# Performance work log

Measured on AMD Instinct MI355X. Metric: run time of the kernel, lower is better.

Reference implementation:

```python
import jax, jax.numpy as jnp
import numpy as np
from jax import lax

D_MODEL = 256
DEPTH = 2
DI = 512        # d_inner = expand * d_model
N = 16          # d_state
DCONV = 4
DTR = 16        # dt_rank = ceil(d_model/16)
BSZ = 32
T = 2048
EPS = 1e-5


def setup_inputs() -> dict:
    key = jax.random.key(0)
    ks = jax.random.split(key, 13)
    s = 0.02
    x = jax.random.normal(ks[0], (BSZ, T, D_MODEL), jnp.float32)
    mask = jax.random.randint(ks[1], (BSZ, T), 0, 2) > 0
    ln_w = 1.0 + 0.1 * jax.random.normal(ks[2], (DEPTH, D_MODEL), jnp.float32)
    ln_b = 0.1 * jax.random.normal(ks[3], (DEPTH, D_MODEL), jnp.float32)
    in_proj_w = s * jax.random.normal(ks[4], (DEPTH, 2 * DI, D_MODEL), jnp.float32)
    conv_w = s * jax.random.normal(ks[5], (DEPTH, DI, DCONV), jnp.float32)
    conv_b = s * jax.random.normal(ks[6], (DEPTH, DI), jnp.float32)
    x_proj_w = s * jax.random.normal(ks[7], (DEPTH, DTR + 2 * N, DI), jnp.float32)
    dt_proj_w = s * jax.random.normal(ks[8], (DEPTH, DI, DTR), jnp.float32)
    dt_proj_b = s * jax.random.normal(ks[9], (DEPTH, DI), jnp.float32)
    # A = -exp(A_log) in (-e^3, -1): stable decaying dynamics
    A_log = jax.random.uniform(ks[10], (DEPTH, DI, N), jnp.float32, 0.0, 3.0)
    skip_D = s * jax.random.normal(ks[11], (DEPTH, DI), jnp.float32)
    out_proj_w = s * jax.random.normal(ks[12], (DEPTH, D_MODEL, DI), jnp.float32)
    return {"x": x, "mask": mask, "ln_w": ln_w, "ln_b": ln_b,
            "in_proj_w": in_proj_w, "conv_w": conv_w, "conv_b": conv_b,
            "x_proj_w": x_proj_w, "dt_proj_w": dt_proj_w, "dt_proj_b": dt_proj_b,
            "A_log": A_log, "skip_D": skip_D, "out_proj_w": out_proj_w}


def _layernorm(x, w, b):
    mu = jnp.mean(x, axis=-1, keepdims=True)
    var = jnp.mean(jnp.square(x - mu), axis=-1, keepdims=True)
    return (x - mu) * lax.rsqrt(var + EPS) * w + b


def _mamba(x, in_proj_w, conv_w, conv_b, x_proj_w, dt_proj_w, dt_proj_b, A_log, skip_D, out_proj_w):
    Bsz, L, _ = x.shape
    xz = jnp.einsum('btd,ed->bte', x, in_proj_w)      # (B,T,2*DI)
    u, z = jnp.split(xz, 2, axis=-1)                  # (B,T,DI) each
    # causal depthwise conv1d, kernel size DCONV
    up = jnp.pad(u, ((0, 0), (DCONV - 1, 0), (0, 0)))
    uc = conv_b
    for k in range(DCONV):
        uc = uc + up[:, k:k + L, :] * conv_w[:, k]
    u = jax.nn.silu(uc)
    x_dbl = jnp.einsum('btd,ed->bte', u, x_proj_w)    # (B,T,DTR+2N)
    dt_in, Bm, Cm = jnp.split(x_dbl, [DTR, DTR + N], axis=-1)
    dt = jax.nn.softplus(jnp.einsum('btr,dr->btd', dt_in, dt_proj_w) + dt_proj_b)  # (B,T,DI)
    A = -jnp.exp(A_log)                               # (DI,N)

    def step(h, inp):
        dt_t, B_t, C_t, u_t = inp                     # (B,DI),(B,N),(B,N),(B,DI)
        dA = jnp.exp(dt_t[..., None] * A)             # (B,DI,N)
        h = dA * h + (dt_t * u_t)[..., None] * B_t[:, None, :]
        y = jnp.einsum('bdn,bn->bd', h, C_t)
        return h, y

    h0 = jnp.zeros((Bsz, DI, N), x.dtype)
    xs = (dt.transpose(1, 0, 2), Bm.transpose(1, 0, 2),
          Cm.transpose(1, 0, 2), u.transpose(1, 0, 2))
    _, ys = lax.scan(step, h0, xs)                    # (T,B,DI)
    y = ys.transpose(1, 0, 2) + u * skip_D
    y = y * jax.nn.silu(z)
    return jnp.einsum('btd,ed->bte', y, out_proj_w)   # (B,T,d_model)


def reference(x, mask, ln_w, ln_b, in_proj_w, conv_w, conv_b, x_proj_w,
              dt_proj_w, dt_proj_b, A_log, skip_D, out_proj_w):
    m = mask[..., None].astype(x.dtype)
    x = x * m
    for i in range(DEPTH):
        h = _mamba(_layernorm(x, ln_w[i], ln_b[i]), in_proj_w[i], conv_w[i],
                   conv_b[i], x_proj_w[i], dt_proj_w[i], dt_proj_b[i],
                   A_log[i], skip_D[i], out_proj_w[i])
        x = (x + h) * m   # dropout in eval mode = identity
    return x
```

## Files before the change

### kernel.cpp

```cpp
#include <hip/hip_runtime.h>
#include <cstdint>

#define LOG2E 1.4426950408889634f
#define BCH 16
#define RC  (BCH * 2048)

typedef __attribute__((ext_vector_type(8))) short short8;
typedef __attribute__((ext_vector_type(4))) float f32x4;
typedef __attribute__((ext_vector_type(4))) unsigned short ush4;
typedef __attribute__((ext_vector_type(8))) unsigned short ush8;

__device__ __forceinline__ float b2f(unsigned short u) {
  union { unsigned int u; float f; } c; c.u = ((unsigned int)u) << 16; return c.f;
}
__device__ __forceinline__ unsigned short f2b(float f) {
  union { float f; unsigned int u; } c; c.f = f;
  unsigned int r = c.u + 0x7FFFu + ((c.u >> 16) & 1u);
  return (unsigned short)(r >> 16);
}
__device__ __forceinline__ float ex2(float x) { return __builtin_amdgcn_exp2f(x); }
__device__ __forceinline__ f32x4 exp2v(f32x4 v) {
  f32x4 r; r.x = ex2(v.x); r.y = ex2(v.y); r.z = ex2(v.z); r.w = ex2(v.w);
  return r;
}

__device__ __forceinline__ f32x4 ld4(const float* p) {
  f32x4 r;
  asm volatile("global_load_dwordx4 %0, %1, off" : "=v"(r) : "v"(p));
  return r;
}

__device__ __forceinline__ void gl2lds16(void* l, const void* g) {
  __builtin_amdgcn_global_load_lds(
      (const __attribute__((address_space(1))) void*)g,
      (__attribute__((address_space(3))) void*)l, 16, 0, 0);
}

__global__ __launch_bounds__(256) void prep_weights(
    const float* __restrict__ inw, const float* __restrict__ xw,
    const float* __restrict__ ow, const float* __restrict__ alog,
    unsigned short* __restrict__ inwb, unsigned short* __restrict__ xwb,
    unsigned short* __restrict__ owb, float* __restrict__ AA) {
  int gid = blockIdx.x * 256 + threadIdx.x;
  const int n_in = 2 * 1024 * 256;
  const int n_x  = 2 * 48 * 512;
  const int n_o  = 2 * 256 * 512;
  const int n_a  = 2 * 512 * 16;
  if (gid < n_in) { inwb[gid] = f2b(inw[gid]); return; }
  gid -= n_in;
  if (gid < n_x) { xwb[gid] = f2b(xw[gid]); return; }
  gid -= n_x;
  if (gid < n_o) { owb[gid] = f2b(ow[gid]); return; }
  gid -= n_o;
  if (gid < n_a) { AA[gid] = -__expf(alog[gid]) * LOG2E; }
}

__global__ __launch_bounds__(256) void mask_x(
    const float* __restrict__ x, const int* __restrict__ mask,
    float* __restrict__ X) {
  int gid = blockIdx.x * 256 + threadIdx.x;
  int row = gid >> 8;
  X[gid] = mask[row] ? x[gid] : 0.f;
}

__global__ __launch_bounds__(256) void ln_fwd(
    const float* __restrict__ X, const float* __restrict__ w,
    const float* __restrict__ b, unsigned short* __restrict__ XN) {
  int wv = threadIdx.x >> 6, ln = threadIdx.x & 63;
  long row = (long)blockIdx.x * 4 + wv;
  f32x4 v = ((const f32x4*)(X + row * 256))[ln];
  float s = v.x + v.y + v.z + v.w;
  float s2 = v.x * v.x + v.y * v.y + v.z * v.z + v.w * v.w;
  #pragma unroll
  for (int o = 32; o > 0; o >>= 1) {
    s += __shfl_xor(s, o, 64);
    s2 += __shfl_xor(s2, o, 64);
  }
  float mu = s * (1.f / 256.f);
  float var = s2 * (1.f / 256.f) - mu * mu;
  float rst = rsqrtf(var + 1e-5f);
  f32x4 wv4 = ((const f32x4*)w)[ln];
  f32x4 bv4 = ((const f32x4*)b)[ln];
  ush4 o4;
  o4.x = f2b((v.x - mu) * rst * wv4.x + bv4.x);
  o4.y = f2b((v.y - mu) * rst * wv4.y + bv4.y);
  o4.z = f2b((v.z - mu) * rst * wv4.z + bv4.z);
  o4.w = f2b((v.w - mu) * rst * wv4.w + bv4.w);
  ((ush4*)(XN + row * 256))[ln] = o4;
}

__global__ __launch_bounds__(256) void gemm128(
    const unsigned short* __restrict__ A, const unsigned short* __restrict__ B,
    unsigned short* __restrict__ OutU, unsigned short* __restrict__ OutZ,
    int N, int K) {
  __shared__ unsigned short As[128 * 32];
  __shared__ unsigned short Bs[128 * 32];
  const int tid = threadIdx.x;
  const int wave = tid >> 6, lane = tid & 63;
  const int lin = blockIdx.x + blockIdx.y * 256;
  const int xcd = lin & 7, idx = lin >> 3;
  const int m0 = (xcd * 32 + (idx >> 3)) * 128;
  const int n0 = (idx & 7) * 128;
  const int wm = (wave >> 1) * 64, wn = (wave & 1) * 64;

  f32x4 acc[4][4];
  #pragma unroll
  for (int i = 0; i < 4; i++)
    #pragma unroll
    for (int j = 0; j < 4; j++)
      #pragma unroll
      for (int r = 0; r < 4; r++) acc[i][j][r] = 0.f;

  const int srow = wave * 32 + (lane >> 2);
  const int skcol = (lane & 3) * 8;
  unsigned short* AsW = &As[srow * 32 + skcol];
  unsigned short* BsW = &Bs[srow * 32 + skcol];
  const unsigned short* Ag = A + (long)(m0 + srow) * K + skcol;
  const unsigned short* Bg = B + (long)(n0 + srow) * K + skcol;

  const int fr = lane & 15, fk = (lane >> 4) * 8;

  for (int k0 = 0; k0 < K; k0 += 32) {
    gl2lds16(AsW,            Ag + k0);
    gl2lds16(AsW + 16 * 32,  Ag + (long)16 * K + k0);
    gl2lds16(BsW,            Bg + k0);
    gl2lds16(BsW + 16 * 32,  Bg + (long)16 * K + k0);
    __syncthreads();
    short8 af[4], bf[4];
    #pragma unroll
    for (int i = 0; i < 4; i++) {
      af[i] = *(const short8*)&As[(wm + i * 16 + fr) * 32 + fk];
      bf[i] = *(const short8*)&Bs[(wn + i * 16 + fr) * 32 + fk];
    }
    #pragma unroll
    for (int i = 0; i < 4; i++)
      #pragma unroll
      for (int j = 0; j < 4; j++)
        acc[i][j] = __builtin_amdgcn_mfma_f32_16x16x32_bf16(af[i], bf[j], acc[i][j], 0, 0, 0);
    __syncthreads();
  }

  const int cl = lane & 15, rq = (lane >> 4) * 4;
  #pragma unroll
  for (int i = 0; i < 4; i++)
    #pragma unroll
    for (int j = 0; j < 4; j++) {
      int col = n0 + wn + j * 16 + cl;
      #pragma unroll
      for (int r = 0; r < 4; r++) {
        int row = m0 + wm + i * 16 + rq + r;
        float v = acc[i][j][r];
        if (col < 512) OutU[(long)row * 512 + col] = f2b(v);
        else           OutZ[(long)row * 512 + (col - 512)] = f2b(v);
      }
    }
}

__global__ __launch_bounds__(256) void gemm64(
    const unsigned short* __restrict__ A, const unsigned short* __restrict__ B,
    const float* __restrict__ Xres, float* __restrict__ OutF,
    const int* __restrict__ mask, int N, int K) {
  __shared__ unsigned short As[64 * 32];
  __shared__ unsigned short Bs[128 * 32];
  const int tid = threadIdx.x;
  const int wave = tid >> 6, lane = tid & 63;
  const int lin = blockIdx.x + blockIdx.y * 512;
  const int xcd = lin & 7, idx = lin >> 3;
  const int m0 = (xcd * 64 + (idx >> 1)) * 64;
  const int n0 = (idx & 1) * 128;
  const int wm = (wave >> 1) * 32, wn = (wave & 1) * 64;

  f32x4 acc[2][4];
  #pragma unroll
  for (int i = 0; i < 2; i++)
    #pragma unroll
    for (int j = 0; j < 4; j++)
      #pragma unroll
      for (int r = 0; r < 4; r++) acc[i][j][r] = 0.f;

  const int srow = wave * 32 + (lane >> 2);
  const int skcol = (lane & 3) * 8;
  unsigned short* AsW = &As[srow * 32 + skcol];
  unsigned short* BsW = &Bs[srow * 32 + skcol];
  const unsigned short* Ag = A + (long)(m0 + srow) * K + skcol;
  const unsigned short* Bg = B + (long)(n0 + srow) * K + skcol;

  const int fr = lane & 15, fk = (lane >> 4) * 8;

  for (int k0 = 0; k0 < K; k0 += 32) {
    if (wave < 2) {
      gl2lds16(AsW,            Ag + k0);
      gl2lds16(AsW + 16 * 32,  Ag + (long)16 * K + k0);
    }
    gl2lds16(BsW,            Bg + k0);
    gl2lds16(BsW + 16 * 32,  Bg + (long)16 * K + k0);
    __syncthreads();
    short8 af[2], bf[4];
    #pragma unroll
    for (int i = 0; i < 2; i++)
      af[i] = *(const short8*)&As[(wm + i * 16 + fr) * 32 + fk];
    #pragma unroll
    for (int j = 0; j < 4; j++)
      bf[j] = *(const short8*)&Bs[(wn + j * 16 + fr) * 32 + fk];
    #pragma unroll
    for (int i = 0; i < 2; i++)
      #pragma unroll
      for (int j = 0; j < 4; j++)
        acc[i][j] = __builtin_amdgcn_mfma_f32_16x16x32_bf16(af[i], bf[j], acc[i][j], 0, 0, 0);
    __syncthreads();
  }

  const int cl = lane & 15, rq = (lane >> 4) * 4;
  #pragma unroll
  for (int i = 0; i < 2; i++)
    #pragma unroll
    for (int j = 0; j < 4; j++) {
      int col = n0 + wn + j * 16 + cl;
      #pragma unroll
      for (int r = 0; r < 4; r++) {
        int row = m0 + wm + i * 16 + rq + r;
        long idx2 = (long)row * N + col;
        OutF[idx2] = Xres[idx2] + (mask[row] ? acc[i][j][r] : 0.f);
      }
    }
}

__global__ __launch_bounds__(256) void gemm_n48(
    const unsigned short* __restrict__ A, const unsigned short* __restrict__ B,
    float* __restrict__ Out, int K) {
  __shared__ unsigned short As[128 * 32];
  __shared__ unsigned short Bs[48 * 32];
  const int tid = threadIdx.x;
  const int wave = tid >> 6, lane = tid & 63;
  const int m0 = blockIdx.x * 128;
  const int wm = wave * 32;

  f32x4 acc[2][3];
  #pragma unroll
  for (int i = 0; i < 2; i++)
    #pragma unroll
    for (int j = 0; j < 3; j++)
      #pragma unroll
      for (int r = 0; r < 4; r++) acc[i][j][r] = 0.f;

  const int srow = wave * 32 + (lane >> 2);
  const int skcol = (lane & 3) * 8;
  unsigned short* AsW = &As[srow * 32 + skcol];
  const unsigned short* Ag = A + (long)(m0 + srow) * K + skcol;
  const int brow = wave * 16 + (lane >> 2);
  unsigned short* BsW = &Bs[brow * 32 + skcol];
  const unsigned short* Bg = B + (long)brow * K + skcol;

  const int fr = lane & 15, fk = (lane >> 4) * 8;

  for (int k0 = 0; k0 < K; k0 += 32) {
    gl2lds16(AsW,           Ag + k0);
    gl2lds16(AsW + 16 * 32, Ag + (long)16 * K + k0);
    if (wave < 3) gl2lds16(BsW, Bg + k0);
    __syncthreads();
    short8 af[2], bf[3];
    #pragma unroll
    for (int i = 0; i < 2; i++)
      af[i] = *(const short8*)&As[(wm + i * 16 + fr) * 32 + fk];
    #pragma unroll
    for (int j = 0; j < 3; j++)
      bf[j] = *(const short8*)&Bs[(j * 16 + fr) * 32 + fk];
    #pragma unroll
    for (int i = 0; i < 2; i++)
      #pragma unroll
      for (int j = 0; j < 3; j++)
        acc[i][j] = __builtin_amdgcn_mfma_f32_16x16x32_bf16(af[i], bf[j], acc[i][j], 0, 0, 0);
    __syncthreads();
  }

  const int cl = lane & 15, rq = (lane >> 4) * 4;
  #pragma unroll
  for (int i = 0; i < 2; i++)
    #pragma unroll
    for (int j = 0; j < 3; j++) {
      int col = j * 16 + cl;
      #pragma unroll
      for (int r = 0; r < 4; r++) {
        int row = m0 + wm + i * 16 + rq + r;
        Out[(long)row * 48 + col] = acc[i][j][r];
      }
    }
}

__global__ __launch_bounds__(256, 4) void conv_silu(
    const unsigned short* __restrict__ Upre, const float* __restrict__ cw,
    const float* __restrict__ cb, unsigned short* __restrict__ U) {
  int gid = blockIdx.x * 256 + threadIdx.x;
  int d8 = gid & 63;
  int row = gid >> 6;
  int t = row & 2047;
  int d0 = d8 * 8;
  f32x4 cwv[8];
  #pragma unroll
  for (int di = 0; di < 8; di++) cwv[di] = ((const f32x4*)(cw + (d0 + di) * 4))[0];
  f32x4 cbv0 = ((const f32x4*)(cb + d0))[0];
  f32x4 cbv1 = ((const f32x4*)(cb + d0))[1];
  float acc[8] = {cbv0.x, cbv0.y, cbv0.z, cbv0.w, cbv1.x, cbv1.y, cbv1.z, cbv1.w};
  #pragma unroll
  for (int k = 0; k < 4; k++) {
    int tt = t + k - 3;
    if (tt >= 0) {
      ush8 uv = *(const ush8*)(Upre + (long)(row + k - 3) * 512 + d0);
      #pragma unroll
      for (int di = 0; di < 8; di++)
        acc[di] = fmaf(b2f(uv[di]), cwv[di][k], acc[di]);
    }
  }
  ush8 o;
  #pragma unroll
  for (int di = 0; di < 8; di++) {
    float sg = 1.f / (1.f + __expf(-acc[di]));
    o[di] = f2b(acc[di] * sg);
  }
  *(ush8*)(U + (long)row * 512 + d0) = o;
}

template<int DTM>
__global__ __launch_bounds__(256, 8) void scan_p1(
    const unsigned short* __restrict__ U, const float* __restrict__ XD,
    const float* __restrict__ AA, const float* __restrict__ dtw,
    const float* __restrict__ dtb, float* __restrict__ HCH,
    float* __restrict__ DTS, _Float16* __restrict__ DTH) {
  int gid = blockIdx.x * 256 + threadIdx.x;
  int d = gid & 511;
  int bc = gid >> 9;
  int c = bc & 63, b = bc >> 6;
  f32x4 aa0 = ld4(AA + d * 16),      aa1 = ld4(AA + d * 16 + 4),
        aa2 = ld4(AA + d * 16 + 8),  aa3 = ld4(AA + d * 16 + 12);
  f32x4 w0 = ld4(dtw + d * 16),      w1 = ld4(dtw + d * 16 + 4),
        w2 = ld4(dtw + d * 16 + 8),  w3 = ld4(dtw + d * 16 + 12);
  asm volatile("s_waitcnt vmcnt(0)"
               : "+v"(aa0), "+v"(aa1), "+v"(aa2), "+v"(aa3),
                 "+v"(w0), "+v"(w1), "+v"(w2), "+v"(w3));
  f32x4 h0 = {0.f,0.f,0.f,0.f}, h1 = h0, h2 = h0, h3 = h0;
  float bias = dtb[d];
  float dts = 0.f;
  int row = b * 2048 + c * 32;
  const unsigned short* Up = U + (long)row * 512 + d;
  _Float16* DTp = DTH + (long)row * 512 + d;
  for (int tt = 0; tt < 32; tt++, row++, Up += 512, DTp += 512) {
    int off = __builtin_amdgcn_readfirstlane(row * 48);
    const f32x4* xs = (const f32x4*)(XD + off);
    f32x4 x0 = xs[0], x1 = xs[1], x2 = xs[2], x3 = xs[3];
    f32x4 B0 = xs[4], B1 = xs[5], B2 = xs[6], B3 = xs[7];
    f32x4 pp = x0 * w0 + x1 * w1 + x2 * w2 + x3 * w3;
    float s = bias + pp.x + pp.y + pp.z + pp.w;
    float e = __expf(-fabsf(s));
    float dt = fmaxf(s, 0.f) + __logf(1.f + e);
    if (DTM) *DTp = (_Float16)dt;
    float du = dt * b2f(*Up);
    h0 = exp2v(dt * aa0) * h0 + du * B0;
    h1 = exp2v(dt * aa1) * h1 + du * B1;
    h2 = exp2v(dt * aa2) * h2 + du * B2;
    h3 = exp2v(dt * aa3) * h3 + du * B3;
    dts += dt;
  }
  f32x4* hp = (f32x4*)(HCH + (long)gid * 16);
  hp[0] = h0; hp[1] = h1; hp[2] = h2; hp[3] = h3;
  DTS[gid] = dts;
}

__global__ __launch_bounds__(256) void scan_p2(
    float* __restrict__ HCH, const float* __restrict__ DTS,
    const float* __restrict__ AA) {
  int gid = blockIdx.x * 256 + threadIdx.x;
  int n = gid & 15;
  int d = (gid >> 4) & 511;
  int b = gid >> 13;
  float aa = AA[d * 16 + n];
  float hrun = 0.f;
  for (int c = 0; c < 64; c++) {
    long base = ((long)b * 64 + c) * 512 + d;
    long idx = base * 16 + n;
    float hend = HCH[idx];
    float P = ex2(DTS[base] * aa);
    HCH[idx] = hrun;
    hrun = fmaf(P, hrun, hend);
  }
}

template<int DTM>
__global__ __launch_bounds__(256, 8) void scan_p3(
    const unsigned short* __restrict__ U, const unsigned short* __restrict__ Z,
    const float* __restrict__ XD, const float* __restrict__ AA,
    const float* __restrict__ dtw, const float* __restrict__ dtb,
    const float* __restrict__ HCH, const float* __restrict__ skD,
    unsigned short* __restrict__ Y, const _Float16* __restrict__ DTH) {
  int gid = blockIdx.x * 256 + threadIdx.x;
  int d = gid & 511;
  int bc = gid >> 9;
  int c = bc & 63, b = bc >> 6;
  f32x4 aa0 = ld4(AA + d * 16),      aa1 = ld4(AA + d * 16 + 4),
        aa2 = ld4(AA + d * 16 + 8),  aa3 = ld4(AA + d * 16 + 12);
  f32x4 w0, w1, w2, w3;
  if (!DTM) {
    w0 = ld4(dtw + d * 16);     w1 = ld4(dtw + d * 16 + 4);
    w2 = ld4(dtw + d * 16 + 8); w3 = ld4(dtw + d * 16 + 12);
    asm volatile("s_waitcnt vmcnt(0)"
                 : "+v"(aa0), "+v"(aa1), "+v"(aa2), "+v"(aa3),
                   "+v"(w0), "+v"(w1), "+v"(w2), "+v"(w3));
  } else {
    asm volatile("s_waitcnt vmcnt(0)"
                 : "+v"(aa0), "+v"(aa1), "+v"(aa2), "+v"(aa3));
  }
  const f32x4* hp = (const f32x4*)(HCH + (long)gid * 16);
  f32x4 h0 = hp[0], h1 = hp[1], h2 = hp[2], h3 = hp[3];
  float bias = DTM ? 0.f : dtb[d];
  float sD = skD[d];
  int row = b * 2048 + c * 32;
  const unsigned short* Up = U + (long)row * 512 + d;
  const unsigned short* Zp = Z + (long)row * 512 + d;
  unsigned short* Yp = Y + (long)row * 512 + d;
  const _Float16* DTp = DTH + (long)row * 512 + d;
  for (int tt = 0; tt < 32; tt++, row++, Up += 512, Zp += 512, Yp += 512, DTp += 512) {
    int off = __builtin_amdgcn_readfirstlane(row * 48);
    const f32x4* xs = (const f32x4*)(XD + off);
    f32x4 B0 = xs[4], B1 = xs[5], B2 = xs[6], B3 = xs[7];
    f32x4 C0 = xs[8], C1 = xs[9], C2 = xs[10], C3 = xs[11];
    float dt;
    if (DTM) {
      dt = (float)*DTp;
    } else {
      f32x4 x0 = xs[0], x1 = xs[1], x2 = xs[2], x3 = xs[3];
      f32x4 pp = x0 * w0 + x1 * w1 + x2 * w2 + x3 * w3;
      float s = bias + pp.x + pp.y + pp.z + pp.w;
      float e = __expf(-fabsf(s));
      dt = fmaxf(s, 0.f) + __logf(1.f + e);
    }
    float u = b2f(*Up);
    float du = dt * u;
    h0 = exp2v(dt * aa0) * h0 + du * B0;
    h1 = exp2v(dt * aa1) * h1 + du * B1;
    h2 = exp2v(dt * aa2) * h2 + du * B2;
    h3 = exp2v(dt * aa3) * h3 + du * B3;
    f32x4 yv = h0 * C0 + h1 * C1 + h2 * C2 + h3 * C3;
    float y = yv.x + yv.y + yv.z + yv.w + u * sD;
    float z = b2f(*Zp);
    float sg = z / (1.f + __expf(-z));
    *Yp = f2b(y * sg);
  }
}

extern "C" void kernel_launch(void* const* d_in, const int* in_sizes, int n_in,
                              void* d_out, int out_size, void* d_ws, size_t ws_size,
                              hipStream_t stream) {
  const float* x        = (const float*)d_in[0];
  const int*   mask     = (const int*)d_in[1];
  const float* ln_w     = (const float*)d_in[2];
  const float* ln_b     = (const float*)d_in[3];
  const float* in_proj  = (const float*)d_in[4];
  const float* conv_w   = (const float*)d_in[5];
  const float* conv_b   = (const float*)d_in[6];
  const float* x_proj   = (const float*)d_in[7];
  const float* dt_w     = (const float*)d_in[8];
  const float* dt_b     = (const float*)d_in[9];
  const float* A_log    = (const float*)d_in[10];
  const float* skip_D   = (const float*)d_in[11];
  const float* out_proj = (const float*)d_in[12];
  float* X = (float*)d_out;

  char* p = (char*)d_ws;
  auto alloc = [&](size_t n) { char* r = p; p += (n + 255) & ~(size_t)255; return r; };
  unsigned short* WBin  = (unsigned short*)alloc((size_t)2 * 1024 * 256 * 2);
  unsigned short* WBx   = (unsigned short*)alloc((size_t)2 * 48 * 512 * 2);
  unsigned short* WBout = (unsigned short*)alloc((size_t)2 * 256 * 512 * 2);
  float*          AA    = (float*)alloc((size_t)2 * 512 * 16 * 4);
  char* R_XN   = alloc((size_t)RC * 256 * 2);
  char* R_UPRE = alloc((size_t)RC * 512 * 2);
  char* R_Z    = alloc((size_t)RC * 512 * 2);
  char* R_U    = alloc((size_t)RC * 512 * 2);
  char* R_DT   = alloc((size_t)RC * 512 * 2);

  unsigned short* XN   = (unsigned short*)R_XN;
  float*          XD   = (float*)R_XN;
  float*          DTS  = (float*)(R_XN + 8388608);
  unsigned short* Upre = (unsigned short*)R_UPRE;
  float*          HCH  = (float*)R_UPRE;
  unsigned short* Z    = (unsigned short*)R_Z;
  unsigned short* U    = (unsigned short*)R_U;
  _Float16*       DTH  = (_Float16*)R_DT;

  const bool use_dt = ws_size >= (size_t)((char*)p - (char*)d_ws);

  prep_weights<<<3328, 256, 0, stream>>>(in_proj, x_proj, out_proj, A_log,
                                         WBin, WBx, WBout, AA);
  mask_x<<<65536, 256, 0, stream>>>(x, mask, X);

  for (int ch = 0; ch < 2; ch++) {
    const long row0 = (long)ch * RC;
    float* Xc = X + row0 * 256;
    const int* maskc = mask + row0;
    for (int i = 0; i < 2; i++) {
      ln_fwd<<<RC / 4, 256, 0, stream>>>(Xc, ln_w + i * 256, ln_b + i * 256, XN);
      gemm128<<<dim3(RC / 128, 8), 256, 0, stream>>>(XN, WBin + i * 262144,
          Upre, Z, 1024, 256);
      conv_silu<<<RC / 4, 256, 0, stream>>>(Upre, conv_w + i * 2048,
          conv_b + i * 512, U);
      gemm_n48<<<RC / 128, 256, 0, stream>>>(U, WBx + i * 24576, XD, 512);
      if (use_dt) {
        scan_p1<1><<<BCH * 128, 256, 0, stream>>>(U, XD, AA + i * 8192,
            dt_w + i * 8192, dt_b + i * 512, HCH, DTS, DTH);
      } else {
        scan_p1<0><<<BCH * 128, 256, 0, stream>>>(U, XD, AA + i * 8192,
            dt_w + i * 8192, dt_b + i * 512, HCH, DTS, DTH);
      }
      scan_p2<<<BCH * 32, 256, 0, stream>>>(HCH, DTS, AA + i * 8192);
      if (use_dt) {
        scan_p3<1><<<BCH * 128, 256, 0, stream>>>(U, Z, XD, AA + i * 8192,
            dt_w + i * 8192, dt_b + i * 512, HCH, skip_D + i * 512, U, DTH);
      } else {
        scan_p3<0><<<BCH * 128, 256, 0, stream>>>(U, Z, XD, AA + i * 8192,
            dt_w + i * 8192, dt_b + i * 512, HCH, skip_D + i * 512, U, DTH);
      }
      gemm64<<<dim3(RC / 64, 2), 256, 0, stream>>>(U, WBout + i * 131072,
          Xc, Xc, maskc, 256, 512);
    }
  }
}
```

Baseline: 1.125 ms.

## Process two scan chunks per thread and fuse masking into first layernorm

```diff
diff --git a/kernel.cpp b/kernel.cpp
--- a/kernel.cpp
+++ b/kernel.cpp
@@ -55,20 +55,41 @@
   if (gid < n_a) { AA[gid] = -__expf(alog[gid]) * LOG2E; }
 }
 
-__global__ __launch_bounds__(256) void mask_x(
-    const float* __restrict__ x, const int* __restrict__ mask,
-    float* __restrict__ X) {
-  int gid = blockIdx.x * 256 + threadIdx.x;
-  int row = gid >> 8;
-  X[gid] = mask[row] ? x[gid] : 0.f;
-}
-
 __global__ __launch_bounds__(256) void ln_fwd(
     const float* __restrict__ X, const float* __restrict__ w,
     const float* __restrict__ b, unsigned short* __restrict__ XN) {
   int wv = threadIdx.x >> 6, ln = threadIdx.x & 63;
   long row = (long)blockIdx.x * 4 + wv;
   f32x4 v = ((const f32x4*)(X + row * 256))[ln];
+  float s = v.x + v.y + v.z + v.w;
+  float s2 = v.x * v.x + v.y * v.y + v.z * v.z + v.w * v.w;
+  #pragma unroll
+  for (int o = 32; o > 0; o >>= 1) {
+    s += __shfl_xor(s, o, 64);
+    s2 += __shfl_xor(s2, o, 64);
+  }
+  float mu = s * (1.f / 256.f);
+  float var = s2 * (1.f / 256.f) - mu * mu;
+  float rst = rsqrtf(var + 1e-5f);
+  f32x4 wv4 = ((const f32x4*)w)[ln];
+  f32x4 bv4 = ((const f32x4*)b)[ln];
+  ush4 o4;
+  o4.x = f2b((v.x - mu) * rst * wv4.x + bv4.x);
+  o4.y = f2b((v.y - mu) * rst * wv4.y + bv4.y);
+  o4.z = f2b((v.z - mu) * rst * wv4.z + bv4.z);
+  o4.w = f2b((v.w - mu) * rst * wv4.w + bv4.w);
+  ((ush4*)(XN + row * 256))[ln] = o4;
+}
+
+__global__ __launch_bounds__(256) void ln_mask_fwd(
+    const float* __restrict__ Xin, const int* __restrict__ mask,
+    const float* __restrict__ w, const float* __restrict__ b,
+    float* __restrict__ Xout, unsigned short* __restrict__ XN) {
+  int wv = threadIdx.x >> 6, ln = threadIdx.x & 63;
+  long row = (long)blockIdx.x * 4 + wv;
+  f32x4 v = ((const f32x4*)(Xin + row * 256))[ln];
+  if (!mask[row]) { v.x = 0.f; v.y = 0.f; v.z = 0.f; v.w = 0.f; }
+  ((f32x4*)(Xout + row * 256))[ln] = v;
   float s = v.x + v.y + v.z + v.w;
   float s2 = v.x * v.x + v.y * v.y + v.z * v.z + v.w * v.w;
   #pragma unroll
@@ -321,15 +342,15 @@
 }
 
 template<int DTM>
-__global__ __launch_bounds__(256, 8) void scan_p1(
+__global__ __launch_bounds__(256, 3) void scan_p1(
     const unsigned short* __restrict__ U, const float* __restrict__ XD,
     const float* __restrict__ AA, const float* __restrict__ dtw,
     const float* __restrict__ dtb, float* __restrict__ HCH,
     float* __restrict__ DTS, _Float16* __restrict__ DTH) {
   int gid = blockIdx.x * 256 + threadIdx.x;
   int d = gid & 511;
-  int bc = gid >> 9;
-  int c = bc & 63, b = bc >> 6;
+  int pc = gid >> 9;
+  int c = pc & 31, b = pc >> 5;
   f32x4 aa0 = ld4(AA + d * 16),      aa1 = ld4(AA + d * 16 + 4),
         aa2 = ld4(AA + d * 16 + 8),  aa3 = ld4(AA + d * 16 + 12);
   f32x4 w0 = ld4(dtw + d * 16),      w1 = ld4(dtw + d * 16 + 4),
@@ -337,32 +358,56 @@
   asm volatile("s_waitcnt vmcnt(0)"
                : "+v"(aa0), "+v"(aa1), "+v"(aa2), "+v"(aa3),
                  "+v"(w0), "+v"(w1), "+v"(w2), "+v"(w3));
-  f32x4 h0 = {0.f,0.f,0.f,0.f}, h1 = h0, h2 = h0, h3 = h0;
+  f32x4 hA0 = {0.f,0.f,0.f,0.f}, hA1 = hA0, hA2 = hA0, hA3 = hA0;
+  f32x4 hB0 = hA0, hB1 = hA0, hB2 = hA0, hB3 = hA0;
   float bias = dtb[d];
-  float dts = 0.f;
-  int row = b * 2048 + c * 32;
-  const unsigned short* Up = U + (long)row * 512 + d;
-  _Float16* DTp = DTH + (long)row * 512 + d;
-  for (int tt = 0; tt < 32; tt++, row++, Up += 512, DTp += 512) {
-    int off = __builtin_amdgcn_readfirstlane(row * 48);
-    const f32x4* xs = (const f32x4*)(XD + off);
-    f32x4 x0 = xs[0], x1 = xs[1], x2 = xs[2], x3 = xs[3];
-    f32x4 B0 = xs[4], B1 = xs[5], B2 = xs[6], B3 = xs[7];
-    f32x4 pp = x0 * w0 + x1 * w1 + x2 * w2 + x3 * w3;
-    float s = bias + pp.x + pp.y + pp.z + pp.w;
-    float e = __expf(-fabsf(s));
-    float dt = fmaxf(s, 0.f) + __logf(1.f + e);
-    if (DTM) *DTp = (_Float16)dt;
-    float du = dt * b2f(*Up);
-    h0 = exp2v(dt * aa0) * h0 + du * B0;
-    h1 = exp2v(dt * aa1) * h1 + du * B1;
-    h2 = exp2v(dt * aa2) * h2 + du * B2;
-    h3 = exp2v(dt * aa3) * h3 + du * B3;
-    dts += dt;
-  }
-  f32x4* hp = (f32x4*)(HCH + (long)gid * 16);
-  hp[0] = h0; hp[1] = h1; hp[2] = h2; hp[3] = h3;
-  DTS[gid] = dts;
+  float dtsA = 0.f, dtsB = 0.f;
+  int rowA = b * 2048 + c * 32;
+  int rowB = rowA + 1024;
+  const unsigned short* UpA = U + (long)rowA * 512 + d;
+  const unsigned short* UpB = U + (long)rowB * 512 + d;
+  _Float16* DTpA = DTH + (long)rowA * 512 + d;
+  _Float16* DTpB = DTH + (long)rowB * 512 + d;
+  for (int tt = 0; tt < 32; tt++) {
+    int offA = __builtin_amdgcn_readfirstlane(rowA * 48);
+    int offB = __builtin_amdgcn_readfirstlane(rowB * 48);
+    const f32x4* xsA = (const f32x4*)(XD + offA);
+    const f32x4* xsB = (const f32x4*)(XD + offB);
+    unsigned short uA = *UpA, uB = *UpB;
+    f32x4 xA0 = xsA[0], xA1 = xsA[1], xA2 = xsA[2], xA3 = xsA[3];
+    f32x4 xB0 = xsB[0], xB1 = xsB[1], xB2 = xsB[2], xB3 = xsB[3];
+    f32x4 ppA = xA0 * w0 + xA1 * w1 + xA2 * w2 + xA3 * w3;
+    f32x4 ppB = xB0 * w0 + xB1 * w1 + xB2 * w2 + xB3 * w3;
+    float sA = bias + ppA.x + ppA.y + ppA.z + ppA.w;
+    float sB = bias + ppB.x + ppB.y + ppB.z + ppB.w;
+    float eA = __expf(-fabsf(sA));
+    float eB = __expf(-fabsf(sB));
+    float dtA = fmaxf(sA, 0.f) + __logf(1.f + eA);
+    float dtB = fmaxf(sB, 0.f) + __logf(1.f + eB);
+    if (DTM) { *DTpA = (_Float16)dtA; *DTpB = (_Float16)dtB; }
+    float duA = dtA * b2f(uA);
+    float duB = dtB * b2f(uB);
+    f32x4 BA0 = xsA[4], BA1 = xsA[5], BA2 = xsA[6], BA3 = xsA[7];
+    f32x4 BB0 = xsB[4], BB1 = xsB[5], BB2 = xsB[6], BB3 = xsB[7];
+    hA0 = exp2v(dtA * aa0) * hA0 + duA * BA0;
+    hB0 = exp2v(dtB * aa0) * hB0 + duB * BB0;
+    hA1 = exp2v(dtA * aa1) * hA1 + duA * BA1;
+    hB1 = exp2v(dtB * aa1) * hB1 + duB * BB1;
+    hA2 = exp2v(dtA * aa2) * hA2 + duA * BA2;
+    hB2 = exp2v(dtB * aa2) * hB2 + duB * BB2;
+    hA3 = exp2v(dtA * aa3) * hA3 + duA * BA3;
+    hB3 = exp2v(dtB * aa3) * hB3 + duB * BB3;
+    dtsA += dtA; dtsB += dtB;
+    rowA++; rowB++; UpA += 512; UpB += 512; DTpA += 512; DTpB += 512;
+  }
+  long gidA = ((long)b * 64 + c) * 512 + d;
+  long gidB = gidA + 32 * 512;
+  f32x4* hpA = (f32x4*)(HCH + gidA * 16);
+  hpA[0] = hA0; hpA[1] = hA1; hpA[2] = hA2; hpA[3] = hA3;
+  f32x4* hpB = (f32x4*)(HCH + gidB * 16);
+  hpB[0] = hB0; hpB[1] = hB1; hpB[2] = hB2; hpB[3] = hB3;
+  DTS[gidA] = dtsA;
+  DTS[gidB] = dtsB;
 }
 
 __global__ __launch_bounds__(256) void scan_p2(
@@ -374,18 +419,29 @@
   int b = gid >> 13;
   float aa = AA[d * 16 + n];
   float hrun = 0.f;
-  for (int c = 0; c < 64; c++) {
-    long base = ((long)b * 64 + c) * 512 + d;
-    long idx = base * 16 + n;
-    float hend = HCH[idx];
-    float P = ex2(DTS[base] * aa);
-    HCH[idx] = hrun;
-    hrun = fmaf(P, hrun, hend);
+  for (int c4 = 0; c4 < 64; c4 += 4) {
+    float he0, he1, he2, he3, P0, P1, P2, P3;
+    long i0, i1, i2, i3;
+    {
+      long base0 = ((long)b * 64 + c4 + 0) * 512 + d;
+      long base1 = ((long)b * 64 + c4 + 1) * 512 + d;
+      long base2 = ((long)b * 64 + c4 + 2) * 512 + d;
+      long base3 = ((long)b * 64 + c4 + 3) * 512 + d;
+      i0 = base0 * 16 + n; i1 = base1 * 16 + n;
+      i2 = base2 * 16 + n; i3 = base3 * 16 + n;
+      he0 = HCH[i0]; he1 = HCH[i1]; he2 = HCH[i2]; he3 = HCH[i3];
+      P0 = ex2(DTS[base0] * aa); P1 = ex2(DTS[base1] * aa);
+      P2 = ex2(DTS[base2] * aa); P3 = ex2(DTS[base3] * aa);
+    }
+    HCH[i0] = hrun; hrun = fmaf(P0, hrun, he0);
+    HCH[i1] = hrun; hrun = fmaf(P1, hrun, he1);
+    HCH[i2] = hrun; hrun = fmaf(P2, hrun, he2);
+    HCH[i3] = hrun; hrun = fmaf(P3, hrun, he3);
   }
 }
 
 template<int DTM>
-__global__ __launch_bounds__(256, 8) void scan_p3(
+__global__ __launch_bounds__(256, 3) void scan_p3(
     const unsigned short* __restrict__ U, const unsigned short* __restrict__ Z,
     const float* __restrict__ XD, const float* __restrict__ AA,
     const float* __restrict__ dtw, const float* __restrict__ dtb,
@@ -393,8 +449,8 @@
     unsigned short* __restrict__ Y, const _Float16* __restrict__ DTH) {
   int gid = blockIdx.x * 256 + threadIdx.x;
   int d = gid & 511;
-  int bc = gid >> 9;
-  int c = bc & 63, b = bc >> 6;
+  int pc = gid >> 9;
+  int c = pc & 31, b = pc >> 5;
   f32x4 aa0 = ld4(AA + d * 16),      aa1 = ld4(AA + d * 16 + 4),
         aa2 = ld4(AA + d * 16 + 8),  aa3 = ld4(AA + d * 16 + 12);
   f32x4 w0, w1, w2, w3;
@@ -408,41 +464,81 @@
     asm volatile("s_waitcnt vmcnt(0)"
                  : "+v"(aa0), "+v"(aa1), "+v"(aa2), "+v"(aa3));
   }
-  const f32x4* hp = (const f32x4*)(HCH + (long)gid * 16);
-  f32x4 h0 = hp[0], h1 = hp[1], h2 = hp[2], h3 = hp[3];
+  long gidA = ((long)b * 64 + c) * 512 + d;
+  long gidB = gidA + 32 * 512;
+  f32x4 hA0, hA1, hA2, hA3, hB0, hB1, hB2, hB3;
+  {
+    const f32x4* hpA = (const f32x4*)(HCH + gidA * 16);
+    hA0 = hpA[0]; hA1 = hpA[1]; hA2 = hpA[2]; hA3 = hpA[3];
+    const f32x4* hpB = (const f32x4*)(HCH + gidB * 16);
+    hB0 = hpB[0]; hB1 = hpB[1]; hB2 = hpB[2]; hB3 = hpB[3];
+  }
   float bias = DTM ? 0.f : dtb[d];
   float sD = skD[d];
-  int row = b * 2048 + c * 32;
-  const unsigned short* Up = U + (long)row * 512 + d;
-  const unsigned short* Zp = Z + (long)row * 512 + d;
-  unsigned short* Yp = Y + (long)row * 512 + d;
-  const _Float16* DTp = DTH + (long)row * 512 + d;
-  for (int tt = 0; tt < 32; tt++, row++, Up += 512, Zp += 512, Yp += 512, DTp += 512) {
-    int off = __builtin_amdgcn_readfirstlane(row * 48);
-    const f32x4* xs = (const f32x4*)(XD + off);
-    f32x4 B0 = xs[4], B1 = xs[5], B2 = xs[6], B3 = xs[7];
-    f32x4 C0 = xs[8], C1 = xs[9], C2 = xs[10], C3 = xs[11];
-    float dt;
+  int rowA = b * 2048 + c * 32;
+  int rowB = rowA + 1024;
+  const unsigned short* UpA = U + (long)rowA * 512 + d;
+  const unsigned short* UpB = U + (long)rowB * 512 + d;
+  const unsigned short* ZpA = Z + (long)rowA * 512 + d;
+  const unsigned short* ZpB = Z + (long)rowB * 512 + d;
+  unsigned short* YpA = Y + (long)rowA * 512 + d;
+  unsigned short* YpB = Y + (long)rowB * 512 + d;
+  const _Float16* DTpA = DTH + (long)rowA * 512 + d;
+  const _Float16* DTpB = DTH + (long)rowB * 512 + d;
+  for (int tt = 0; tt < 32; tt++) {
+    int offA = __builtin_amdgcn_readfirstlane(rowA * 48);
+    int offB = __builtin_amdgcn_readfirstlane(rowB * 48);
+    const f32x4* xsA = (const f32x4*)(XD + offA);
+    const f32x4* xsB = (const f32x4*)(XD + offB);
+    unsigned short uA16 = *UpA, uB16 = *UpB;
+    unsigned short zA16 = *ZpA, zB16 = *ZpB;
+    float dtA, dtB;
     if (DTM) {
-      dt = (float)*DTp;
+      dtA = (float)*DTpA;
+      dtB = (float)*DTpB;
     } else {
-      f32x4 x0 = xs[0], x1 = xs[1], x2 = xs[2], x3 = xs[3];
-      f32x4 pp = x0 * w0 + x1 * w1 + x2 * w2 + x3 * w3;
-      float s = bias + pp.x + pp.y + pp.z + pp.w;
-      float e = __expf(-fabsf(s));
-      dt = fmaxf(s, 0.f) + __logf(1.f + e);
-    }
-    float u = b2f(*Up);
-    float du = dt * u;
-    h0 = exp2v(dt * aa0) * h0 + du * B0;
-    h1 = exp2v(dt * aa1) * h1 + du * B1;
-    h2 = exp2v(dt * aa2) * h2 + du * B2;
-    h3 = exp2v(dt * aa3) * h3 + du * B3;
-    f32x4 yv = h0 * C0 + h1 * C1 + h2 * C2 + h3 * C3;
-    float y = yv.x + yv.y + yv.z + yv.w + u * sD;
-    float z = b2f(*Zp);
-    float sg = z / (1.f + __expf(-z));
-    *Yp = f2b(y * sg);
+      f32x4 xA0 = xsA[0], xA1 = xsA[1], xA2 = xsA[2], xA3 = xsA[3];
+      f32x4 ppA = xA0 * w0 + xA1 * w1 + xA2 * w2 + xA3 * w3;
+      float sA = bias + ppA.x + ppA.y + ppA.z + ppA.w;
+      float eA = __expf(-fabsf(sA));
+      dtA = fmaxf(sA, 0.f) + __logf(1.f + eA);
+      f32x4 xB0 = xsB[0], xB1 = xsB[1], xB2 = xsB[2], xB3 = xsB[3];
+      f32x4 ppB = xB0 * w0 + xB1 * w1 + xB2 * w2 + xB3 * w3;
+      float sB = bias + ppB.x + ppB.y + ppB.z + ppB.w;
+      float eB = __expf(-fabsf(sB));
+      dtB = fmaxf(sB, 0.f) + __logf(1.f + eB);
+    }
+    float uA = b2f(uA16), uB = b2f(uB16);
+    float duA = dtA * uA, duB = dtB * uB;
+    {
+      f32x4 BA0 = xsA[4], BA1 = xsA[5], BA2 = xsA[6], BA3 = xsA[7];
+      f32x4 CA0 = xsA[8], CA1 = xsA[9], CA2 = xsA[10], CA3 = xsA[11];
+      hA0 = exp2v(dtA * aa0) * hA0 + duA * BA0;
+      hA1 = exp2v(dtA * aa1) * hA1 + duA * BA1;
+      hA2 = exp2v(dtA * aa2) * hA2 + duA * BA2;
+      hA3 = exp2v(dtA * aa3) * hA3 + duA * BA3;
+      f32x4 yv = hA0 * CA0 + hA1 * CA1 + hA2 * CA2 + hA3 * CA3;
+      float y = yv.x + yv.y + yv.z + yv.w + uA * sD;
+      float z = b2f(zA16);
+      float sg = z / (1.f + __expf(-z));
+      *YpA = f2b(y * sg);
+    }
+    {
+      f32x4 BB0 = xsB[4], BB1 = xsB[5], BB2 = xsB[6], BB3 = xsB[7];
+      f32x4 CB0 = xsB[8], CB1 = xsB[9], CB2 = xsB[10], CB3 = xsB[11];
+      hB0 = exp2v(dtB * aa0) * hB0 + duB * BB0;
+      hB1 = exp2v(dtB * aa1) * hB1 + duB * BB1;
+      hB2 = exp2v(dtB * aa2) * hB2 + duB * BB2;
+      hB3 = exp2v(dtB * aa3) * hB3 + duB * BB3;
+      f32x4 yv = hB0 * CB0 + hB1 * CB1 + hB2 * CB2 + hB3 * CB3;
+      float y = yv.x + yv.y + yv.z + yv.w + uB * sD;
+      float z = b2f(zB16);
+      float sg = z / (1.f + __expf(-z));
+      *YpB = f2b(y * sg);
+    }
+    rowA++; rowB++;
+    UpA += 512; UpB += 512; ZpA += 512; ZpB += 512;
+    YpA += 512; YpB += 512; DTpA += 512; DTpB += 512;
   }
 }
 
@@ -489,32 +585,36 @@
 
   prep_weights<<<3328, 256, 0, stream>>>(in_proj, x_proj, out_proj, A_log,
                                          WBin, WBx, WBout, AA);
-  mask_x<<<65536, 256, 0, stream>>>(x, mask, X);
 
   for (int ch = 0; ch < 2; ch++) {
     const long row0 = (long)ch * RC;
     float* Xc = X + row0 * 256;
     const int* maskc = mask + row0;
     for (int i = 0; i < 2; i++) {
-      ln_fwd<<<RC / 4, 256, 0, stream>>>(Xc, ln_w + i * 256, ln_b + i * 256, XN);
+      if (i == 0) {
+        ln_mask_fwd<<<RC / 4, 256, 0, stream>>>(x + row0 * 256, maskc,
+            ln_w, ln_b, Xc, XN);
+      } else {
+        ln_fwd<<<RC / 4, 256, 0, stream>>>(Xc, ln_w + i * 256, ln_b + i * 256, XN);
+      }
       gemm128<<<dim3(RC / 128, 8), 256, 0, stream>>>(XN, WBin + i * 262144,
           Upre, Z, 1024, 256);
       conv_silu<<<RC / 4, 256, 0, stream>>>(Upre, conv_w + i * 2048,
           conv_b + i * 512, U);
       gemm_n48<<<RC / 128, 256, 0, stream>>>(U, WBx + i * 24576, XD, 512);
       if (use_dt) {
-        scan_p1<1><<<BCH * 128, 256, 0, stream>>>(U, XD, AA + i * 8192,
+        scan_p1<1><<<BCH * 64, 256, 0, stream>>>(U, XD, AA + i * 8192,
             dt_w + i * 8192, dt_b + i * 512, HCH, DTS, DTH);
       } else {
-        scan_p1<0><<<BCH * 128, 256, 0, stream>>>(U, XD, AA + i * 8192,
+        scan_p1<0><<<BCH * 64, 256, 0, stream>>>(U, XD, AA + i * 8192,
             dt_w + i * 8192, dt_b + i * 512, HCH, DTS, DTH);
       }
       scan_p2<<<BCH * 32, 256, 0, stream>>>(HCH, DTS, AA + i * 8192);
       if (use_dt) {
-        scan_p3<1><<<BCH * 128, 256, 0, stream>>>(U, Z, XD, AA + i * 8192,
+        scan_p3<1><<<BCH * 64, 256, 0, stream>>>(U, Z, XD, AA + i * 8192,
             dt_w + i * 8192, dt_b + i * 512, HCH, skip_D + i * 512, U, DTH);
       } else {
-        scan_p3<0><<<BCH * 128, 256, 0, stream>>>(U, Z, XD, AA + i * 8192,
+        scan_p3<0><<<BCH * 64, 256, 0, stream>>>(U, Z, XD, AA + i * 8192,
             dt_w + i * 8192, dt_b + i * 512, HCH, skip_D + i * 512, U, DTH);
       }
       gemm64<<<dim3(RC / 64, 2), 256, 0, stream>>>(U, WBout + i * 131072,
```

New measurement: 1.137 ms. About the same (+1.1%).
